# Optimization experiments

Measured on AMD Instinct MI355X. Metric: run time of the kernel, lower is better.

The kernel has to match this reference:

```python
import jax, jax.numpy as jnp
import numpy as np

LN_EPS = 1e-5


def _ln(x, g, b):
    mu = jnp.mean(x, -1, keepdims=True)
    xc = x - mu
    inv = jax.lax.rsqrt(jnp.mean(xc * xc, -1, keepdims=True) + LN_EPS)
    return xc * inv * g + b


def _subm_conv(x, nbr, W, b):
    # Submanifold 3D conv via rulebook gather-GEMM-accumulate.
    # x: [N, Cin], nbr: [N, K] neighbor row ids (-1 = missing), W: [K, Cin, Cout], b: [Cout]
    N = x.shape[0]
    xp = jnp.concatenate([x, jnp.zeros((1, x.shape[1]), x.dtype)], 0)  # sentinel zero row
    idx = jnp.where(nbr < 0, N, nbr)  # missing neighbors -> zero row
    acc0 = jnp.zeros((N, W.shape[-1]), x.dtype) + b
    def body(acc, xs):
        i, Wk = xs  # i: [N], Wk: [Cin, Cout]
        return acc + xp[i] @ Wk, None
    acc, _ = jax.lax.scan(body, acc0, (idx.T, W))
    return acc


def _blk1(x, W, b, g, be):  # 1x1x1 SubMConv + LN + ReLU
    return jax.nn.relu(_ln(x @ W + b, g, be))


def _blk3(x, nbr, W, b, g, be):  # 3x3x3 SubMConv + LN + ReLU
    return jax.nn.relu(_ln(_subm_conv(x, nbr, W, b), g, be))


def setup_inputs() -> dict:
    rng = np.random.default_rng(0)
    B, D, Npb, K = 2, 160, 131072, 27
    dim, half = 64, 32
    # Build random sparse voxel set and the rulebook (neighbor table) like spconv does.
    lookup = np.full((B, D, D, D), -1, np.int64)
    coords = np.zeros((B * Npb, 3), np.int64)
    for b in range(B):
        lin = np.sort(rng.choice(D * D * D, size=Npb, replace=False))
        z, y, x = np.unravel_index(lin, (D, D, D))
        rows = np.arange(b * Npb, (b + 1) * Npb)
        lookup[b, z, y, x] = rows
        coords[rows] = np.stack([z, y, x], 1)
    bidx = np.repeat(np.arange(B), Npb)
    offs = np.stack(np.meshgrid(np.arange(-1, 2), np.arange(-1, 2), np.arange(-1, 2), indexing="ij"), -1).reshape(K, 3)
    nz = coords[:, None, :] + offs[None]  # [N, K, 3]
    valid = ((nz >= 0) & (nz < D)).all(-1)
    nzc = np.clip(nz, 0, D - 1)
    nbr = lookup[bidx[:, None], nzc[..., 0], nzc[..., 1], nzc[..., 2]]
    nbr = np.where(valid, nbr, -1).astype(np.int32)

    key = jax.random.key(0)
    ks = iter(jax.random.split(key, 16))
    f32 = jnp.float32
    d = {"voxel_features": jax.random.normal(next(ks), (B * Npb, dim), f32),
         "nbr_idx": jnp.asarray(nbr)}
    def lnp(c):
        return jnp.ones((c,), f32), jnp.zeros((c,), f32)
    d["W1"] = 0.05 * jax.random.normal(next(ks), (dim, dim), f32); d["b1"] = jnp.zeros((dim,), f32); d["g1"], d["be1"] = lnp(dim)
    d["W2"] = 0.05 * jax.random.normal(next(ks), (dim, dim), f32); d["b2"] = jnp.zeros((dim,), f32); d["g2"], d["be2"] = lnp(dim)
    d["W3"] = 0.05 * jax.random.normal(next(ks), (K, dim, half), f32); d["b3"] = jnp.zeros((half,), f32); d["g3"], d["be3"] = lnp(half)
    d["W4"] = 0.05 * jax.random.normal(next(ks), (K, half, half), f32); d["b4"] = jnp.zeros((half,), f32); d["g4"], d["be4"] = lnp(half)
    d["W5"] = 0.05 * jax.random.normal(next(ks), (K, half, half), f32); d["b5"] = jnp.zeros((half,), f32); d["g5"], d["be5"] = lnp(half)
    d["W6"] = 0.05 * jax.random.normal(next(ks), (K, half, half), f32); d["b6"] = jnp.zeros((half,), f32); d["g6"], d["be6"] = lnp(half)
    d["W7"] = 0.05 * jax.random.normal(next(ks), (4 * dim, dim), f32); d["b7"] = jnp.zeros((dim,), f32); d["g7"], d["be7"] = lnp(dim)
    return d


def reference(voxel_features, nbr_idx,
              W1, b1, g1, be1, W2, b2, g2, be2,
              W3, b3, g3, be3, W4, b4, g4, be4,
              W5, b5, g5, be5, W6, b6, g6, be6,
              W7, b7, g7, be7):
    x = voxel_features
    f1 = _blk1(x, W1, b1, g1, be1)
    f2 = _blk1(x, W2, b2, g2, be2)
    feats = [f1, f2]
    f2 = _blk3(f2, nbr_idx, W3, b3, g3, be3); feats.append(f2)
    f2 = _blk3(f2, nbr_idx, W4, b4, g4, be4); feats.append(f2)
    f2 = _blk3(f2, nbr_idx, W5, b5, g5, be5); feats.append(f2)
    f2 = _blk3(f2, nbr_idx, W6, b6, g6, be6); feats.append(f2)
    cat = jnp.concatenate(feats, -1)  # [N, 4*dim]
    return _blk1(cat, W7, b7, g7, be7)
```

## Files before the change

kernel.cpp:

```cpp
#include <hip/hip_runtime.h>

typedef __attribute__((ext_vector_type(4))) float  float4_;
typedef __attribute__((ext_vector_type(8))) short  short8;
typedef __attribute__((ext_vector_type(8))) __bf16 bf16x8;

__device__ inline unsigned short f2bf(float f) {
    unsigned u = __builtin_bit_cast(unsigned, f);
    u += 0x7FFFu + ((u >> 16) & 1u);
    return (unsigned short)(u >> 16);
}

__device__ inline float4_ mfma16(bf16x8 a, bf16x8 b, float4_ c) {
    return __builtin_amdgcn_mfma_f32_16x16x32_bf16(a, b, c, 0, 0, 0);
}

__device__ inline void packW_one(const float* __restrict__ src, unsigned short* __restrict__ dst,
                                 int cin, int cout, int e) {
    int f = e >> 9, i = e & 511, lane = i >> 3, t = i & 7;
    int ntn = cout >> 4, ctn = cin >> 5;
    int nt = f % ntn;
    int rest = f / ntn;
    int ct = rest % ctn;
    int k = rest / ctn;
    int c = ct * 32 + (lane >> 4) * 8 + t;
    int j = nt * 16 + (lane & 15);
    dst[e] = f2bf(src[(k * cin + c) * cout + j]);
}

__global__ void pack_all_kernel(
    const float* __restrict__ W1, const float* __restrict__ W2,
    const float* __restrict__ W3, const float* __restrict__ W4,
    const float* __restrict__ W5, const float* __restrict__ W6,
    const float* __restrict__ W7,
    unsigned short* cat, unsigned short* Wp12, unsigned short* Wp3,
    unsigned short* Wp4, unsigned short* Wp5, unsigned short* Wp6,
    unsigned short* Wp7, int N) {
    int e = blockIdx.x * 256 + threadIdx.x;
    if (e < 8192) {
        int f = e >> 9, i = e & 511, lane = i >> 3, t = i & 7;
        int nt = f & 7, ct = f >> 3;
        int c = ct * 32 + (lane >> 4) * 8 + t;
        int j = nt * 16 + (lane & 15);
        float v = (j < 64) ? W1[c * 64 + j] : W2[c * 64 + (j - 64)];
        Wp12[e] = f2bf(v);
        return;
    }
    e -= 8192;
    if (e < 55296) { packW_one(W3, Wp3, 64, 32, e); return; }
    e -= 55296;
    if (e < 27648) { packW_one(W4, Wp4, 32, 32, e); return; }
    e -= 27648;
    if (e < 27648) { packW_one(W5, Wp5, 32, 32, e); return; }
    e -= 27648;
    if (e < 27648) { packW_one(W6, Wp6, 32, 32, e); return; }
    e -= 27648;
    if (e < 16384) { packW_one(W7, Wp7, 256, 64, e); return; }
    e -= 16384;
    if (e < 128) ((unsigned*)(cat + (size_t)N * 256))[e] = 0;
}

__global__ __launch_bounds__(256) void plan_kernel(const int* __restrict__ nbr,
                                                   unsigned int* __restrict__ kmask) {
    int tid = threadIdx.x, lane = tid & 63, wv = tid >> 6;
    int l15 = lane & 15, q = lane >> 4;
    int t = (blockIdx.x * 4 + wv) * 4 + q;
    const int* np = nbr + ((long)t * 16 + l15) * 27;
    unsigned m = 0;
#pragma unroll
    for (int k = 0; k < 27; k++) {
        int v = np[k];
        unsigned long long bal = __ballot(v >= 0);
        if ((bal >> (q * 16)) & 0xFFFFull) m |= (1u << k);
    }
    if (l15 == 0) kmask[t] = m;
}

__global__ __launch_bounds__(256) void blk12_kernel(
    const float* __restrict__ x, unsigned short* cat,
    const unsigned short* __restrict__ Wp,
    const float* __restrict__ b1, const float* __restrict__ g1, const float* __restrict__ be1,
    const float* __restrict__ b2, const float* __restrict__ g2, const float* __restrict__ be2) {
    int tid = threadIdx.x, lane = tid & 63, wv = tid >> 6;
    int l15 = lane & 15, q = lane >> 4;
    long base = ((long)blockIdx.x * 4 + wv) * 16;

    float4_ acc[8];
#pragma unroll
    for (int i = 0; i < 8; i++) acc[i] = (float4_){0.f, 0.f, 0.f, 0.f};

#pragma unroll
    for (int kt = 0; kt < 2; kt++) {
        const float* xp = x + (base + l15) * 64 + kt * 32 + q * 8;
        float4_ f0 = *(const float4_*)xp;
        float4_ f1 = *(const float4_*)(xp + 4);
        short8 as;
        as[0] = (short)f2bf(f0[0]); as[1] = (short)f2bf(f0[1]);
        as[2] = (short)f2bf(f0[2]); as[3] = (short)f2bf(f0[3]);
        as[4] = (short)f2bf(f1[0]); as[5] = (short)f2bf(f1[1]);
        as[6] = (short)f2bf(f1[2]); as[7] = (short)f2bf(f1[3]);
        bf16x8 a = __builtin_bit_cast(bf16x8, as);
        const unsigned short* wp = Wp + (size_t)kt * 8 * 512;
#pragma unroll
        for (int nt = 0; nt < 8; nt++) {
            bf16x8 w = *(const bf16x8*)(wp + nt * 512 + lane * 8);
            acc[nt] = mfma16(a, w, acc[nt]);
        }
    }

    float bc[8], gc[8], bec[8];
#pragma unroll
    for (int nt = 0; nt < 8; nt++) {
        int j = nt * 16 + l15;
        if (j < 64) { bc[nt] = b1[j]; gc[nt] = g1[j]; bec[nt] = be1[j]; }
        else        { bc[nt] = b2[j - 64]; gc[nt] = g2[j - 64]; bec[nt] = be2[j - 64]; }
    }

#pragma unroll
    for (int r = 0; r < 4; r++) {
        long row = base + q * 4 + r;
        float v[8], s0 = 0.f, s1 = 0.f, q0 = 0.f, q1 = 0.f;
#pragma unroll
        for (int nt = 0; nt < 4; nt++) { v[nt] = acc[nt][r] + bc[nt]; s0 += v[nt]; q0 += v[nt] * v[nt]; }
#pragma unroll
        for (int nt = 4; nt < 8; nt++) { v[nt] = acc[nt][r] + bc[nt]; s1 += v[nt]; q1 += v[nt] * v[nt]; }
#pragma unroll
        for (int m = 1; m < 16; m <<= 1) {
            s0 += __shfl_xor(s0, m); q0 += __shfl_xor(q0, m);
            s1 += __shfl_xor(s1, m); q1 += __shfl_xor(q1, m);
        }
        float mu0 = s0 * (1.f / 64), var0 = q0 * (1.f / 64) - mu0 * mu0, inv0 = rsqrtf(var0 + 1e-5f);
        float mu1 = s1 * (1.f / 64), var1 = q1 * (1.f / 64) - mu1 * mu1, inv1 = rsqrtf(var1 + 1e-5f);
        unsigned short* cp = cat + row * 256;
#pragma unroll
        for (int nt = 0; nt < 4; nt++) {
            float y = fmaxf((v[nt] - mu0) * inv0 * gc[nt] + bec[nt], 0.f);
            cp[nt * 16 + l15] = f2bf(y);
        }
#pragma unroll
        for (int nt = 4; nt < 8; nt++) {
            float y = fmaxf((v[nt] - mu1) * inv1 * gc[nt] + bec[nt], 0.f);
            cp[nt * 16 + l15] = f2bf(y);
        }
    }
}

template <int CT, int D>
__global__ __launch_bounds__(256) void conv_kernel(
    unsigned short* cat, const int* __restrict__ nbr,
    const unsigned int* __restrict__ kmask,
    const unsigned short* __restrict__ Wp,
    const float* __restrict__ bb, const float* __restrict__ gg, const float* __restrict__ bee,
    int in_off, int out_off, int N) {
    int tid = threadIdx.x, lane = tid & 63, wv = tid >> 6;
    int l15 = lane & 15, q = lane >> 4;

    int cpx = (int)(gridDim.x >> 3);
    int sb = ((int)blockIdx.x & 7) * cpx + ((int)blockIdx.x >> 3);
    int t = sb * 4 + wv;
    long base = (long)t * 16;

    unsigned m = __builtin_amdgcn_readfirstlane(kmask[t]);

    float4_ acc[2];
    acc[0] = (float4_){0.f, 0.f, 0.f, 0.f};
    acc[1] = (float4_){0.f, 0.f, 0.f, 0.f};

    const unsigned short* catp = cat + in_off + q * 8;
    const unsigned short* wl = Wp + lane * 8;
    const int* np = nbr + (base + l15) * 27;

    bf16x8 f[D + 1][CT];
    bf16x8 wr[3][CT][2];
    int rawi[3];

    int raw0[D + 2];
#pragma unroll
    for (int j = 0; j < D + 2; j++) raw0[j] = (m >> j & 1u) ? np[j] : -1;

#pragma unroll
    for (int kk = 0; kk < 2; kk++) {
        if (m >> kk & 1u) {
#pragma unroll
            for (int ct = 0; ct < CT; ct++)
#pragma unroll
                for (int nt = 0; nt < 2; nt++)
                    wr[kk][ct][nt] =
                        *(const bf16x8*)(wl + ((size_t)((kk * CT + ct) * 2 + nt)) * 512);
        }
    }

#pragma unroll
    for (int j = 0; j < D; j++) {
        if (m >> j & 1u) {
            int v = raw0[j];
            size_t s = (size_t)(v < 0 ? N : v);
#pragma unroll
            for (int ct = 0; ct < CT; ct++)
                f[j][ct] = *(const bf16x8*)(catp + s * 256 + ct * 32);
        }
    }
    rawi[D % 3] = raw0[D];
    rawi[(D + 1) % 3] = raw0[D + 1];

#pragma unroll
    for (int k = 0; k < 27; k++) {
        if (k + 2 < 27 && (m >> (k + 2) & 1u)) {
#pragma unroll
            for (int ct = 0; ct < CT; ct++)
#pragma unroll
                for (int nt = 0; nt < 2; nt++)
                    wr[(k + 2) % 3][ct][nt] =
                        *(const bf16x8*)(wl + ((size_t)(((k + 2) * CT + ct) * 2 + nt)) * 512);
        }
        if (k + D < 27 && (m >> (k + D) & 1u)) {
            int v = rawi[(k + D) % 3];
            size_t s = (size_t)(v < 0 ? N : v);
#pragma unroll
            for (int ct = 0; ct < CT; ct++)
                f[(k + D) % (D + 1)][ct] = *(const bf16x8*)(catp + s * 256 + ct * 32);
        }
        if (k + D + 2 < 27 && (m >> (k + D + 2) & 1u)) {
            rawi[(k + D + 2) % 3] = np[k + D + 2];
        }
        if (m >> k & 1u) {
#pragma unroll
            for (int ct = 0; ct < CT; ct++) {
                bf16x8 w0 = wr[k % 3][ct][0];
                bf16x8 w1 = wr[k % 3][ct][1];
                acc[0] = mfma16(f[k % (D + 1)][ct], w0, acc[0]);
                acc[1] = mfma16(f[k % (D + 1)][ct], w1, acc[1]);
            }
        }
    }

    float b0c = bb[l15], b1c = bb[16 + l15];
    float g0c = gg[l15], g1c = gg[16 + l15];
    float be0c = bee[l15], be1c = bee[16 + l15];

#pragma unroll
    for (int r = 0; r < 4; r++) {
        long row = base + q * 4 + r;
        float v0 = acc[0][r] + b0c;
        float v1 = acc[1][r] + b1c;
        float s = v0 + v1, sq = v0 * v0 + v1 * v1;
#pragma unroll
        for (int mh = 1; mh < 16; mh <<= 1) { s += __shfl_xor(s, mh); sq += __shfl_xor(sq, mh); }
        float mu = s * (1.f / 32), var = sq * (1.f / 32) - mu * mu, inv = rsqrtf(var + 1e-5f);
        float y0 = fmaxf((v0 - mu) * inv * g0c + be0c, 0.f);
        float y1 = fmaxf((v1 - mu) * inv * g1c + be1c, 0.f);
        unsigned short* cp = cat + row * 256 + out_off;
        cp[l15] = f2bf(y0);
        cp[16 + l15] = f2bf(y1);
    }
}

__global__ __launch_bounds__(256) void blk7_kernel(
    const unsigned short* __restrict__ cat, const unsigned short* __restrict__ Wp,
    const float* __restrict__ b, const float* __restrict__ g, const float* __restrict__ be,
    float* __restrict__ out) {
    int tid = threadIdx.x, lane = tid & 63, wv = tid >> 6;
    int l15 = lane & 15, q = lane >> 4;
    long base = ((long)blockIdx.x * 4 + wv) * 16;

    float4_ acc[4];
#pragma unroll
    for (int i = 0; i < 4; i++) acc[i] = (float4_){0.f, 0.f, 0.f, 0.f};

#pragma unroll
    for (int kt = 0; kt < 8; kt++) {
        bf16x8 a = *(const bf16x8*)(cat + (base + l15) * 256 + kt * 32 + q * 8);
        const unsigned short* wp = Wp + (size_t)kt * 4 * 512;
#pragma unroll
        for (int nt = 0; nt < 4; nt++) {
            bf16x8 w = *(const bf16x8*)(wp + nt * 512 + lane * 8);
            acc[nt] = mfma16(a, w, acc[nt]);
        }
    }

    float bc[4], gc[4], bec[4];
#pragma unroll
    for (int nt = 0; nt < 4; nt++) {
        int j = nt * 16 + l15;
        bc[nt] = b[j]; gc[nt] = g[j]; bec[nt] = be[j];
    }

#pragma unroll
    for (int r = 0; r < 4; r++) {
        long row = base + q * 4 + r;
        float v[4], s = 0.f, sq = 0.f;
#pragma unroll
        for (int nt = 0; nt < 4; nt++) { v[nt] = acc[nt][r] + bc[nt]; s += v[nt]; sq += v[nt] * v[nt]; }
#pragma unroll
        for (int m = 1; m < 16; m <<= 1) { s += __shfl_xor(s, m); sq += __shfl_xor(sq, m); }
        float mu = s * (1.f / 64), var = sq * (1.f / 64) - mu * mu, inv = rsqrtf(var + 1e-5f);
#pragma unroll
        for (int nt = 0; nt < 4; nt++) {
            float y = fmaxf((v[nt] - mu) * inv * gc[nt] + bec[nt], 0.f);
            out[row * 64 + nt * 16 + l15] = y;
        }
    }
}

extern "C" void kernel_launch(void* const* d_in, const int* in_sizes, int n_in,
                              void* d_out, int out_size, void* d_ws, size_t ws_size,
                              hipStream_t stream) {
    const int N = in_sizes[0] / 64;

    const float* x   = (const float*)d_in[0];
    const int*   nbr = (const int*)d_in[1];
    const float* W1 = (const float*)d_in[2];
    const float* b1 = (const float*)d_in[3];
    const float* g1 = (const float*)d_in[4];
    const float* be1 = (const float*)d_in[5];
    const float* W2 = (const float*)d_in[6];
    const float* b2 = (const float*)d_in[7];
    const float* g2 = (const float*)d_in[8];
    const float* be2 = (const float*)d_in[9];
    const float* W3 = (const float*)d_in[10];
    const float* b3 = (const float*)d_in[11];
    const float* g3 = (const float*)d_in[12];
    const float* be3 = (const float*)d_in[13];
    const float* W4 = (const float*)d_in[14];
    const float* b4 = (const float*)d_in[15];
    const float* g4 = (const float*)d_in[16];
    const float* be4 = (const float*)d_in[17];
    const float* W5 = (const float*)d_in[18];
    const float* b5 = (const float*)d_in[19];
    const float* g5 = (const float*)d_in[20];
    const float* be5 = (const float*)d_in[21];
    const float* W6 = (const float*)d_in[22];
    const float* b6 = (const float*)d_in[23];
    const float* g6 = (const float*)d_in[24];
    const float* be6 = (const float*)d_in[25];
    const float* W7 = (const float*)d_in[26];
    const float* b7 = (const float*)d_in[27];
    const float* g7 = (const float*)d_in[28];
    const float* be7 = (const float*)d_in[29];

    unsigned short* ws   = (unsigned short*)d_ws;
    unsigned short* cat  = ws;
    unsigned short* Wp12 = cat + (size_t)(N + 1) * 256;
    unsigned short* Wp3  = Wp12 + 8192;
    unsigned short* Wp4  = Wp3 + 55296;
    unsigned short* Wp5  = Wp4 + 27648;
    unsigned short* Wp6  = Wp5 + 27648;
    unsigned short* Wp7  = Wp6 + 27648;
    unsigned int*   kmask = (unsigned int*)(Wp7 + 16384);

    pack_all_kernel<<<637, 256, 0, stream>>>(W1, W2, W3, W4, W5, W6, W7,
                                             cat, Wp12, Wp3, Wp4, Wp5, Wp6, Wp7, N);
    plan_kernel<<<N / 16 / 16, 256, 0, stream>>>(nbr, kmask);

    blk12_kernel<<<N / 64, 256, 0, stream>>>(x, cat, Wp12, b1, g1, be1, b2, g2, be2);
    conv_kernel<2, 3><<<N / 64, 256, 0, stream>>>(cat, nbr, kmask, Wp3, b3, g3, be3, 64, 128, N);
    conv_kernel<1, 4><<<N / 64, 256, 0, stream>>>(cat, nbr, kmask, Wp4, b4, g4, be4, 128, 160, N);
    conv_kernel<1, 4><<<N / 64, 256, 0, stream>>>(cat, nbr, kmask, Wp5, b5, g5, be5, 160, 192, N);
    conv_kernel<1, 4><<<N / 64, 256, 0, stream>>>(cat, nbr, kmask, Wp6, b6, g6, be6, 192, 224, N);
    blk7_kernel<<<N / 64, 256, 0, stream>>>(cat, Wp7, b7, g7, be7, (float*)d_out);
}
```

Baseline: 471.5 us.

## Issue all 27 neighbor gathers upfront instead of a rolling prefetch window

The conv kernel now loads all 27 neighbor indices and issues all 27 feature gathers before the MFMA loop, replacing the small D-deep rolling prefetch. Weights are prefetched three taps ahead in a 4-slot ring. For the 64-channel input layer, the two 32-channel halves are processed in two passes, reloading the second half per tap as the first is consumed. The goal is more memory-level parallelism to hide gather latency. The cost is much higher VGPR pressure, which may lower occupancy, and unconditional index loads for masked taps.

Result: no change. 467.6 us (-0.8%).

```diff
diff --git a/kernel.cpp b/kernel.cpp
--- a/kernel.cpp
+++ b/kernel.cpp
@@ -144,7 +144,7 @@
     }
 }
 
-template <int CT, int D>
+template <int CT>
 __global__ __launch_bounds__(256) void conv_kernel(
     unsigned short* cat, const int* __restrict__ nbr,
     const unsigned int* __restrict__ kmask,
@@ -169,66 +169,70 @@
     const unsigned short* wl = Wp + lane * 8;
     const int* np = nbr + (base + l15) * 27;
 
-    bf16x8 f[D + 1][CT];
-    bf16x8 wr[3][CT][2];
-    int rawi[3];
-
-    int raw0[D + 2];
-#pragma unroll
-    for (int j = 0; j < D + 2; j++) raw0[j] = (m >> j & 1u) ? np[j] : -1;
-
-#pragma unroll
-    for (int kk = 0; kk < 2; kk++) {
-        if (m >> kk & 1u) {
-#pragma unroll
-            for (int ct = 0; ct < CT; ct++)
+    int raw[27];
+#pragma unroll
+    for (int k = 0; k < 27; k++) raw[k] = np[k];
+
+    bf16x8 f[27];
+    bf16x8 wr[4][2];
+
+#pragma unroll
+    for (int k = 0; k < 27; k++) {
+        if (m >> k & 1u) {
+            int v = raw[k];
+            size_t s = (size_t)(v < 0 ? N : v);
+            f[k] = *(const bf16x8*)(catp + s * 256);
+        }
+    }
+
+#pragma unroll
+    for (int j = 0; j < 3; j++) {
+        if (m >> j & 1u) {
+#pragma unroll
+            for (int nt = 0; nt < 2; nt++)
+                wr[j][nt] = *(const bf16x8*)(wl + ((size_t)((j * CT + 0) * 2 + nt)) * 512);
+        }
+    }
+
+#pragma unroll
+    for (int k = 0; k < 27; k++) {
+        if (k + 3 < 27 && (m >> (k + 3) & 1u)) {
+#pragma unroll
+            for (int nt = 0; nt < 2; nt++)
+                wr[(k + 3) & 3][nt] =
+                    *(const bf16x8*)(wl + ((size_t)(((k + 3) * CT + 0) * 2 + nt)) * 512);
+        }
+        if (m >> k & 1u) {
+            acc[0] = mfma16(f[k], wr[k & 3][0], acc[0]);
+            acc[1] = mfma16(f[k], wr[k & 3][1], acc[1]);
+            if (CT == 2) {
+                int v = raw[k];
+                size_t s = (size_t)(v < 0 ? N : v);
+                f[k] = *(const bf16x8*)(catp + s * 256 + 32);
+            }
+        }
+    }
+
+    if (CT == 2) {
+#pragma unroll
+        for (int j = 0; j < 3; j++) {
+            if (m >> j & 1u) {
 #pragma unroll
                 for (int nt = 0; nt < 2; nt++)
-                    wr[kk][ct][nt] =
-                        *(const bf16x8*)(wl + ((size_t)((kk * CT + ct) * 2 + nt)) * 512);
-        }
-    }
-
-#pragma unroll
-    for (int j = 0; j < D; j++) {
-        if (m >> j & 1u) {
-            int v = raw0[j];
-            size_t s = (size_t)(v < 0 ? N : v);
-#pragma unroll
-            for (int ct = 0; ct < CT; ct++)
-                f[j][ct] = *(const bf16x8*)(catp + s * 256 + ct * 32);
-        }
-    }
-    rawi[D % 3] = raw0[D];
-    rawi[(D + 1) % 3] = raw0[D + 1];
-
-#pragma unroll
-    for (int k = 0; k < 27; k++) {
-        if (k + 2 < 27 && (m >> (k + 2) & 1u)) {
-#pragma unroll
-            for (int ct = 0; ct < CT; ct++)
+                    wr[j][nt] = *(const bf16x8*)(wl + ((size_t)((j * 2 + 1) * 2 + nt)) * 512);
+            }
+        }
+#pragma unroll
+        for (int k = 0; k < 27; k++) {
+            if (k + 3 < 27 && (m >> (k + 3) & 1u)) {
 #pragma unroll
                 for (int nt = 0; nt < 2; nt++)
-                    wr[(k + 2) % 3][ct][nt] =
-                        *(const bf16x8*)(wl + ((size_t)(((k + 2) * CT + ct) * 2 + nt)) * 512);
-        }
-        if (k + D < 27 && (m >> (k + D) & 1u)) {
-            int v = rawi[(k + D) % 3];
-            size_t s = (size_t)(v < 0 ? N : v);
-#pragma unroll
-            for (int ct = 0; ct < CT; ct++)
-                f[(k + D) % (D + 1)][ct] = *(const bf16x8*)(catp + s * 256 + ct * 32);
-        }
-        if (k + D + 2 < 27 && (m >> (k + D + 2) & 1u)) {
-            rawi[(k + D + 2) % 3] = np[k + D + 2];
-        }
-        if (m >> k & 1u) {
-#pragma unroll
-            for (int ct = 0; ct < CT; ct++) {
-                bf16x8 w0 = wr[k % 3][ct][0];
-                bf16x8 w1 = wr[k % 3][ct][1];
-                acc[0] = mfma16(f[k % (D + 1)][ct], w0, acc[0]);
-                acc[1] = mfma16(f[k % (D + 1)][ct], w1, acc[1]);
+                    wr[(k + 3) & 3][nt] =
+                        *(const bf16x8*)(wl + ((size_t)(((k + 3) * 2 + 1) * 2 + nt)) * 512);
+            }
+            if (m >> k & 1u) {
+                acc[0] = mfma16(f[k], wr[k & 3][0], acc[0]);
+                acc[1] = mfma16(f[k], wr[k & 3][1], acc[1]);
             }
         }
     }
@@ -352,9 +356,9 @@
     plan_kernel<<<N / 16 / 16, 256, 0, stream>>>(nbr, kmask);
 
     blk12_kernel<<<N / 64, 256, 0, stream>>>(x, cat, Wp12, b1, g1, be1, b2, g2, be2);
-    conv_kernel<2, 3><<<N / 64, 256, 0, stream>>>(cat, nbr, kmask, Wp3, b3, g3, be3, 64, 128, N);
-    conv_kernel<1, 4><<<N / 64, 256, 0, stream>>>(cat, nbr, kmask, Wp4, b4, g4, be4, 128, 160, N);
-    conv_kernel<1, 4><<<N / 64, 256, 0, stream>>>(cat, nbr, kmask, Wp5, b5, g5, be5, 160, 192, N);
-    conv_kernel<1, 4><<<N / 64, 256, 0, stream>>>(cat, nbr, kmask, Wp6, b6, g6, be6, 192, 224, N);
+    conv_kernel<2><<<N / 64, 256, 0, stream>>>(cat, nbr, kmask, Wp3, b3, g3, be3, 64, 128, N);
+    conv_kernel<1><<<N / 64, 256, 0, stream>>>(cat, nbr, kmask, Wp4, b4, g4, be4, 128, 160, N);
+    conv_kernel<1><<<N / 64, 256, 0, stream>>>(cat, nbr, kmask, Wp5, b5, g5, be5, 160, 192, N);
+    conv_kernel<1><<<N / 64, 256, 0, stream>>>(cat, nbr, kmask, Wp6, b6, g6, be6, 192, 224, N);
     blk7_kernel<<<N / 64, 256, 0, stream>>>(cat, Wp7, b7, g7, be7, (float*)d_out);
 }
```
